# Performance work log

Hardware: AMD Instinct MI355X
Metric: run time of the kernel (lower is better)

Reference implementation:

```python
import jax, jax.numpy as jnp
import numpy as np

B, S, HID = 2, 1024, 4096
NH, NKV, D = 32, 8, 128
G = NH // NKV            # query heads per KV head (GQA group size)
WINDOW = 512             # sliding window
ROPE_BASE = 10000.0
NEG = -1e30


def setup_inputs() -> dict:
    key = jax.random.key(0)
    k0, k1, k2, k3, k4 = jax.random.split(key, 5)
    hidden_states = jax.random.normal(k0, (B, S, HID), jnp.float32)
    # rotate-half RoPE tables, width = head_dim
    inv_freq = 1.0 / (ROPE_BASE ** (jnp.arange(0, D, 2, dtype=jnp.float32) / D))
    freqs = jnp.outer(jnp.arange(S, dtype=jnp.float32), inv_freq)
    emb = jnp.concatenate([freqs, freqs], axis=-1)  # [S, D]
    cos, sin = jnp.cos(emb), jnp.sin(emb)
    qkv_out = (NH + 2 * NKV) * D  # fused QKV: 6144
    w_qkv = jax.random.normal(k1, (qkv_out, HID), jnp.float32) / np.sqrt(HID).astype(np.float32)
    b_qkv = jax.random.normal(k2, (qkv_out,), jnp.float32) * 0.01
    w_o = jax.random.normal(k3, (HID, NH * D), jnp.float32) / np.sqrt(NH * D).astype(np.float32)
    b_o = jax.random.normal(k4, (HID,), jnp.float32) * 0.01
    return dict(hidden_states=hidden_states, cos=cos, sin=sin,
                w_qkv=w_qkv, b_qkv=b_qkv, w_o=w_o, b_o=b_o)


def _rotate_half(x):
    x1, x2 = jnp.split(x, 2, axis=-1)
    return jnp.concatenate([-x2, x1], axis=-1)


def reference(hidden_states, cos, sin, w_qkv, b_qkv, w_o, b_o):
    # fused QKV projection (with bias, per attention_bias=True)
    qkv = jnp.einsum('bsh,oh->bso', hidden_states, w_qkv) + b_qkv
    q = qkv[..., : NH * D].reshape(B, S, NKV, G, D)
    k = qkv[..., NH * D : (NH + NKV) * D].reshape(B, S, NKV, D)
    v = qkv[..., (NH + NKV) * D :].reshape(B, S, NKV, D)
    # rotate-half RoPE
    c = cos[None, :, None, :]  # [1,S,1,D]
    s = sin[None, :, None, :]
    q = q * c[..., None, :] + _rotate_half(q) * s[..., None, :]
    k = k * c + _rotate_half(k) * s
    # GQA attention: scores [B, NKV, G, Sq, Sk]
    scores = jnp.einsum('bqkgd,bskd->bkgqs', q, k) / np.sqrt(D).astype(np.float32)
    i = jnp.arange(S)[:, None]
    j = jnp.arange(S)[None, :]
    mask = (j <= i) & (i - j < WINDOW)  # causal + sliding window
    scores = jnp.where(mask, scores, NEG)
    p = jax.nn.softmax(scores, axis=-1)
    attn = jnp.einsum('bkgqs,bskd->bqkgd', p, v).reshape(B, S, NH * D)
    return jnp.einsum('bsd,hd->bsh', attn, w_o) + b_o
```

## Files before the change

kernel.cpp:

```cpp
#include <hip/hip_runtime.h>
#include <hip/hip_bf16.h>

#define B_      2
#define S_      1024
#define HID     4096
#define NH      32
#define NKV     8
#define D_      128
#define G_      4
#define WINDOW  512
#define QKV_OUT 6144
#define M_TOT   2048
#define CH      32
#define VSTR    40

typedef __bf16 bf16x8 __attribute__((ext_vector_type(8)));
typedef float  f32x4  __attribute__((ext_vector_type(4)));
typedef unsigned short u16x8 __attribute__((ext_vector_type(8)));

#define AS1 __attribute__((address_space(1)))
#define AS3 __attribute__((address_space(3)))

static __device__ __forceinline__ float bf2f(unsigned short u) {
    union { unsigned int i; float f; } v; v.i = ((unsigned int)u) << 16; return v.f;
}
static __device__ __forceinline__ unsigned short f2bf(float f) {
    union { float f; unsigned int i; } v; v.f = f;
    unsigned int x = v.i;
    return (unsigned short)((x + 0x7fffu + ((x >> 16) & 1u)) >> 16);
}
static __device__ __forceinline__ void gl2lds16(const void* g, void* l) {
    __builtin_amdgcn_global_load_lds((const AS1 void*)g, (AS3 void*)l, 16, 0, 0);
}

__global__ __launch_bounds__(256)
void conv_f32_bf16(const float* __restrict__ src, unsigned short* __restrict__ dst, int n8)
{
    int i = blockIdx.x * 256 + threadIdx.x;
    if (i >= n8) return;
    const float* p = src + (size_t)i * 8;
    float4 f0 = *(const float4*)p;
    float4 f1 = *(const float4*)(p + 4);
    u16x8 h;
    h[0]=f2bf(f0.x); h[1]=f2bf(f0.y); h[2]=f2bf(f0.z); h[3]=f2bf(f0.w);
    h[4]=f2bf(f1.x); h[5]=f2bf(f1.y); h[6]=f2bf(f1.z); h[7]=f2bf(f1.w);
    *(u16x8*)&dst[(size_t)i * 8] = h;
}

template<bool C_BF16>
__global__ __launch_bounds__(256)
void gemm_bf16_bt(const unsigned short* __restrict__ A,
                  const unsigned short* __restrict__ Bw,
                  const float* __restrict__ bias,
                  void* __restrict__ Cv,
                  int M, int N, int K)
{
    __shared__ unsigned short As[128 * 32];
    __shared__ unsigned short Bs[128 * 32];

    const int tid  = threadIdx.x;
    const int m0   = blockIdx.y * 128;
    const int n0   = blockIdx.x * 128;
    const int wave = tid >> 6, lane = tid & 63;
    const int wm   = (wave >> 1) * 64;
    const int wn   = (wave & 1) * 64;
    const int lm   = lane & 15, quad = lane >> 4;

    f32x4 acc[4][4] = {};

    for (int k0 = 0; k0 < K; k0 += 32) {
        __syncthreads();
        #pragma unroll
        for (int p = 0; p < 2; ++p) {
            int chunk = tid + p * 256;
            int row   = chunk >> 2;
            int off   = (chunk & 3) * 8;
            gl2lds16(&A [(size_t)(m0 + row) * K + k0 + off], &As[chunk * 8]);
            gl2lds16(&Bw[(size_t)(n0 + row) * K + k0 + off], &Bs[chunk * 8]);
        }
        __syncthreads();

        bf16x8 afr[4], bfr[4];
        #pragma unroll
        for (int i = 0; i < 4; ++i)
            afr[i] = *(const bf16x8*)&As[(wm + i * 16 + lm) * 32 + quad * 8];
        #pragma unroll
        for (int j = 0; j < 4; ++j)
            bfr[j] = *(const bf16x8*)&Bs[(wn + j * 16 + lm) * 32 + quad * 8];

        #pragma unroll
        for (int i = 0; i < 4; ++i)
            #pragma unroll
            for (int j = 0; j < 4; ++j)
                acc[i][j] = __builtin_amdgcn_mfma_f32_16x16x32_bf16(afr[i], bfr[j], acc[i][j], 0, 0, 0);
    }

    #pragma unroll
    for (int j = 0; j < 4; ++j) {
        int col = n0 + wn + j * 16 + lm;
        float bv = bias[col];
        #pragma unroll
        for (int i = 0; i < 4; ++i) {
            int rowb = m0 + wm + i * 16 + quad * 4;
            #pragma unroll
            for (int r = 0; r < 4; ++r) {
                float val = acc[i][j][r] + bv;
                if (C_BF16)
                    ((unsigned short*)Cv)[(size_t)(rowb + r) * N + col] = f2bf(val);
                else
                    ((float*)Cv)[(size_t)(rowb + r) * N + col] = val;
            }
        }
    }
}

template<bool A_BF16, bool C_BF16>
__global__ __launch_bounds__(256)
void gemm_bt_bias(const void* __restrict__ Av,
                  const float* __restrict__ Bw,
                  const float* __restrict__ bias,
                  void* __restrict__ Cv,
                  int M, int N, int K)
{
    __shared__ unsigned short As[128 * 40];
    __shared__ unsigned short Bs[128 * 40];

    const int tid  = threadIdx.x;
    const int m0   = blockIdx.y * 128;
    const int n0   = blockIdx.x * 128;
    const int wave = tid >> 6, lane = tid & 63;
    const int wm   = (wave >> 1) * 64;
    const int wn   = (wave & 1) * 64;
    const int lm   = lane & 15, quad = lane >> 4;

    f32x4 acc[4][4] = {};

    for (int k0 = 0; k0 < K; k0 += 32) {
        __syncthreads();
        #pragma unroll
        for (int c = 0; c < 2; ++c) {
            int chunk = tid + c * 256;
            int row   = chunk >> 2;
            int off   = (chunk & 3) * 8;
            if (A_BF16) {
                *(u16x8*)&As[row * 40 + off] =
                    *(const u16x8*)&((const unsigned short*)Av)[(size_t)(m0 + row) * K + k0 + off];
            } else {
                const float* ap = &((const float*)Av)[(size_t)(m0 + row) * K + k0 + off];
                float4 f0 = *(const float4*)ap;
                float4 f1 = *(const float4*)(ap + 4);
                u16x8 h;
                h[0]=f2bf(f0.x); h[1]=f2bf(f0.y); h[2]=f2bf(f0.z); h[3]=f2bf(f0.w);
                h[4]=f2bf(f1.x); h[5]=f2bf(f1.y); h[6]=f2bf(f1.z); h[7]=f2bf(f1.w);
                *(u16x8*)&As[row * 40 + off] = h;
            }
            {
                const float* bp = &Bw[(size_t)(n0 + row) * K + k0 + off];
                float4 f0 = *(const float4*)bp;
                float4 f1 = *(const float4*)(bp + 4);
                u16x8 h;
                h[0]=f2bf(f0.x); h[1]=f2bf(f0.y); h[2]=f2bf(f0.z); h[3]=f2bf(f0.w);
                h[4]=f2bf(f1.x); h[5]=f2bf(f1.y); h[6]=f2bf(f1.z); h[7]=f2bf(f1.w);
                *(u16x8*)&Bs[row * 40 + off] = h;
            }
        }
        __syncthreads();

        bf16x8 afr[4], bfr[4];
        #pragma unroll
        for (int i = 0; i < 4; ++i)
            afr[i] = *(const bf16x8*)&As[(wm + i * 16 + lm) * 40 + quad * 8];
        #pragma unroll
        for (int j = 0; j < 4; ++j)
            bfr[j] = *(const bf16x8*)&Bs[(wn + j * 16 + lm) * 40 + quad * 8];

        #pragma unroll
        for (int i = 0; i < 4; ++i)
            #pragma unroll
            for (int j = 0; j < 4; ++j)
                acc[i][j] = __builtin_amdgcn_mfma_f32_16x16x32_bf16(afr[i], bfr[j], acc[i][j], 0, 0, 0);
    }

    #pragma unroll
    for (int j = 0; j < 4; ++j) {
        int col = n0 + wn + j * 16 + lm;
        float bv = bias[col];
        #pragma unroll
        for (int i = 0; i < 4; ++i) {
            int rowb = m0 + wm + i * 16 + quad * 4;
            #pragma unroll
            for (int r = 0; r < 4; ++r) {
                float val = acc[i][j][r] + bv;
                if (C_BF16)
                    ((unsigned short*)Cv)[(size_t)(rowb + r) * N + col] = f2bf(val);
                else
                    ((float*)Cv)[(size_t)(rowb + r) * N + col] = val;
            }
        }
    }
}

__global__ __launch_bounds__(256)
void rope_kernel(unsigned short* __restrict__ qkv,
                 const float* __restrict__ cosb,
                 const float* __restrict__ sinb)
{
    int t    = blockIdx.x * 256 + threadIdx.x;
    int d    = t & 63;
    int rest = t >> 6;
    int head = rest % 40;
    int m    = rest / 40;
    int s    = m & (S_ - 1);
    int obase = (head < NH) ? head * D_ : HID + (head - NH) * D_;
    size_t base = (size_t)m * QKV_OUT + obase;

    float x1 = bf2f(qkv[base + d]);
    float x2 = bf2f(qkv[base + d + 64]);
    float c1 = cosb[s * D_ + d];
    float s1 = sinb[s * D_ + d];
    float c2 = cosb[s * D_ + d + 64];
    float s2 = sinb[s * D_ + d + 64];
    qkv[base + d]      = f2bf(x1 * c1 - x2 * s1);
    qkv[base + d + 64] = f2bf(x2 * c2 + x1 * s2);
}

__global__ __launch_bounds__(256)
void attn_mfma(const unsigned short* __restrict__ qkv,
               unsigned short* __restrict__ attn)
{
    __shared__ unsigned short Kl[CH * 136];
    __shared__ unsigned short Vt[128 * VSTR];
    __shared__ unsigned short Pl[4][16 * 40];

    const int tid  = threadIdx.x;
    const int wave = tid >> 6, lane = tid & 63;
    const int lm   = lane & 15, quad = lane >> 4;
    const int h    = blockIdx.y;
    const int b    = blockIdx.z;
    const int kvh  = h >> 2;
    const int r0b  = blockIdx.x * 64;
    const int rw0  = r0b + wave * 16;

    const size_t qkv_b = (size_t)b * S_ * QKV_OUT;
    const float SCL = 0.12751974f;

    bf16x8 qf[4];
    {
        const unsigned short* qrow = qkv + qkv_b + (size_t)(rw0 + lm) * QKV_OUT + h * D_ + quad * 8;
        #pragma unroll
        for (int kb = 0; kb < 4; ++kb)
            qf[kb] = *(const bf16x8*)(qrow + kb * 32);
    }

    f32x4 O[8] = {};
    float mrow[4] = {-1e30f, -1e30f, -1e30f, -1e30f};
    float lrow[4] = {0.f, 0.f, 0.f, 0.f};

    const int c0   = max(0, r0b - (WINDOW - 1)) & ~(CH - 1);
    const int cend = r0b + 64 - CH;

    for (int c = c0; c <= cend; c += CH) {
        __syncthreads();
        #pragma unroll
        for (int p = 0; p < 2; ++p) {
            int idx = tid + p * 256;
            int row = idx >> 4;
            int d0  = (idx & 15) * 8;
            *(u16x8*)&Kl[row * 136 + d0] =
                *(const u16x8*)(qkv + qkv_b + (size_t)(c + row) * QKV_OUT + HID + kvh * D_ + d0);
        }
        {
            int r2 = (tid & 15) * 2;
            int d0 = (tid >> 4) * 8;
            const unsigned short* vg = qkv + qkv_b + (size_t)(c + r2) * QKV_OUT + HID + NKV * D_ + kvh * D_ + d0;
            u16x8 va = *(const u16x8*)vg;
            u16x8 vb = *(const u16x8*)(vg + QKV_OUT);
            #pragma unroll
            for (int e = 0; e < 8; ++e) {
                unsigned int pack = (unsigned int)va[e] | ((unsigned int)vb[e] << 16);
                *(unsigned int*)&Vt[(d0 + e) * VSTR + r2] = pack;
            }
        }
        __syncthreads();

        if (c + CH - 1 < rw0 - (WINDOW - 1) || c > rw0 + 15) continue;

        f32x4 s0 = {}, s1 = {};
        #pragma unroll
        for (int kb = 0; kb < 4; ++kb) {
            bf16x8 b0 = *(const bf16x8*)&Kl[lm * 136 + kb * 32 + quad * 8];
            bf16x8 b1 = *(const bf16x8*)&Kl[(16 + lm) * 136 + kb * 32 + quad * 8];
            s0 = __builtin_amdgcn_mfma_f32_16x16x32_bf16(qf[kb], b0, s0, 0, 0, 0);
            s1 = __builtin_amdgcn_mfma_f32_16x16x32_bf16(qf[kb], b1, s1, 0, 0, 0);
        }

        const int j0 = c + lm, j1 = c + 16 + lm;
        float alpha[4];
        #pragma unroll
        for (int r = 0; r < 4; ++r) {
            int row = rw0 + quad * 4 + r;
            float t0 = (j0 <= row && row - j0 < WINDOW) ? s0[r] : -3.0e38f;
            float t1 = (j1 <= row && row - j1 < WINDOW) ? s1[r] : -3.0e38f;
            float cm = fmaxf(t0, t1);
            #pragma unroll
            for (int o = 8; o >= 1; o >>= 1) cm = fmaxf(cm, __shfl_xor(cm, o, 16));
            float mnew = fmaxf(mrow[r], cm);
            float al   = exp2f((mrow[r] - mnew) * SCL);
            float p0   = exp2f((t0 - mnew) * SCL);
            float p1   = exp2f((t1 - mnew) * SCL);
            float rs   = p0 + p1;
            #pragma unroll
            for (int o = 8; o >= 1; o >>= 1) rs += __shfl_xor(rs, o, 16);
            mrow[r] = mnew;
            lrow[r] = lrow[r] * al + rs;
            alpha[r] = al;
            Pl[wave][(quad * 4 + r) * 40 + lm]      = f2bf(p0);
            Pl[wave][(quad * 4 + r) * 40 + 16 + lm] = f2bf(p1);
        }

        #pragma unroll
        for (int nt = 0; nt < 8; ++nt)
            #pragma unroll
            for (int r = 0; r < 4; ++r)
                O[nt][r] *= alpha[r];

        bf16x8 pa = *(const bf16x8*)&Pl[wave][lm * 40 + quad * 8];
        #pragma unroll
        for (int nt = 0; nt < 8; ++nt) {
            bf16x8 vbf = *(const bf16x8*)&Vt[(nt * 16 + lm) * VSTR + quad * 8];
            O[nt] = __builtin_amdgcn_mfma_f32_16x16x32_bf16(pa, vbf, O[nt], 0, 0, 0);
        }
    }

    float il[4];
    #pragma unroll
    for (int r = 0; r < 4; ++r) il[r] = 1.0f / lrow[r];
    #pragma unroll
    for (int nt = 0; nt < 8; ++nt)
        #pragma unroll
        for (int r = 0; r < 4; ++r) {
            int row = rw0 + quad * 4 + r;
            attn[(size_t)(b * S_ + row) * (NH * D_) + h * D_ + nt * 16 + lm] = f2bf(O[nt][r] * il[r]);
        }
}

extern "C" void kernel_launch(void* const* d_in, const int* in_sizes, int n_in,
                              void* d_out, int out_size, void* d_ws, size_t ws_size,
                              hipStream_t stream)
{
    const float* hidden = (const float*)d_in[0];
    const float* cosb   = (const float*)d_in[1];
    const float* sinb   = (const float*)d_in[2];
    const float* w_qkv  = (const float*)d_in[3];
    const float* b_qkv  = (const float*)d_in[4];
    const float* w_o    = (const float*)d_in[5];
    const float* b_o    = (const float*)d_in[6];
    float* out = (float*)d_out;

    unsigned char* ws = (unsigned char*)d_ws;
    const size_t QKV_B  = (size_t)M_TOT * QKV_OUT * 2;
    const size_t ATTN_B = (size_t)M_TOT * HID * 2;
    const size_t HB_B   = (size_t)M_TOT * HID * 2;
    const size_t WQ_B   = (size_t)QKV_OUT * HID * 2;
    const size_t WO_B   = (size_t)HID * HID * 2;
    const size_t NEED   = QKV_B + ATTN_B + HB_B + WQ_B;

    unsigned short* qkv_ws  = (unsigned short*)(ws);
    unsigned short* attn_ws = (unsigned short*)(ws + QKV_B);

    dim3 blk(256);

    if (ws_size >= NEED && WO_B <= HB_B + WQ_B) {
        unsigned short* hb = (unsigned short*)(ws + QKV_B + ATTN_B);
        unsigned short* wq = (unsigned short*)(ws + QKV_B + ATTN_B + HB_B);
        unsigned short* wo = (unsigned short*)(ws + QKV_B + ATTN_B);

        int n8h = M_TOT * HID / 8;
        int n8q = QKV_OUT * HID / 8;
        int n8o = HID * HID / 8;
        conv_f32_bf16<<<dim3((n8h + 255) / 256), blk, 0, stream>>>(hidden, hb, n8h);
        conv_f32_bf16<<<dim3((n8q + 255) / 256), blk, 0, stream>>>(w_qkv, wq, n8q);
        gemm_bf16_bt<true><<<dim3(QKV_OUT / 128, M_TOT / 128), blk, 0, stream>>>(
            hb, wq, b_qkv, qkv_ws, M_TOT, QKV_OUT, HID);
        rope_kernel<<<dim3((M_TOT * 40 * 64) / 256), blk, 0, stream>>>(qkv_ws, cosb, sinb);
        conv_f32_bf16<<<dim3((n8o + 255) / 256), blk, 0, stream>>>(w_o, wo, n8o);
        attn_mfma<<<dim3(S_ / 64, NH, B_), blk, 0, stream>>>(qkv_ws, attn_ws);
        gemm_bf16_bt<false><<<dim3(HID / 128, M_TOT / 128), blk, 0, stream>>>(
            attn_ws, wo, b_o, out, M_TOT, HID, NH * D_);
    } else {
        gemm_bt_bias<false, true><<<dim3(QKV_OUT / 128, M_TOT / 128), blk, 0, stream>>>(
            hidden, w_qkv, b_qkv, qkv_ws, M_TOT, QKV_OUT, HID);
        rope_kernel<<<dim3((M_TOT * 40 * 64) / 256), blk, 0, stream>>>(qkv_ws, cosb, sinb);
        attn_mfma<<<dim3(S_ / 64, NH, B_), blk, 0, stream>>>(qkv_ws, attn_ws);
        gemm_bt_bias<true, false><<<dim3(HID / 128, M_TOT / 128), blk, 0, stream>>>(
            attn_ws, w_o, b_o, out, M_TOT, HID, NH * D_);
    }
}
```

Measured before the change: 552.1 us.

## Use 256x256 eight-phase pipelined bf16 GEMM for the QKV projection

Adds a new 512-thread GEMM kernel with 256x256 output tiles, 64-wide K steps, double-buffered LDS filled by direct global-to-LDS loads, an XOR swizzle, and loads for later K tiles interleaved across four MFMA phases with explicit waitcnt and barriers. It replaces the 128x128 GEMM only for the QKV projection and is meant to raise data reuse and hide global memory latency behind MFMA work. The grid shrinks to 24x8 = 192 blocks, which may underfill the 256 CUs, and the hand-tuned waitcnt counts are fragile.

New measurement: 551.4 us. About the same (-0.1%).

```diff
diff --git a/kernel.cpp b/kernel.cpp
--- a/kernel.cpp
+++ b/kernel.cpp
@@ -45,6 +45,159 @@
     h[0]=f2bf(f0.x); h[1]=f2bf(f0.y); h[2]=f2bf(f0.z); h[3]=f2bf(f0.w);
     h[4]=f2bf(f1.x); h[5]=f2bf(f1.y); h[6]=f2bf(f1.z); h[7]=f2bf(f1.w);
     *(u16x8*)&dst[(size_t)i * 8] = h;
+}
+
+#define PHASE_TAIL(MT0, MT1)                                                           \
+    __builtin_amdgcn_sched_barrier(0);                                                 \
+    __builtin_amdgcn_s_barrier();                                                      \
+    asm volatile("s_waitcnt lgkmcnt(0)" ::: "memory");                                 \
+    __builtin_amdgcn_sched_barrier(0);                                                 \
+    __builtin_amdgcn_s_setprio(1);                                                     \
+    _Pragma("unroll")                                                                  \
+    for (int nt = 0; nt < 4; ++nt) {                                                   \
+        acc[MT0][nt] = __builtin_amdgcn_mfma_f32_16x16x32_bf16(a0[0], b[nt][0], acc[MT0][nt], 0, 0, 0); \
+        acc[MT0][nt] = __builtin_amdgcn_mfma_f32_16x16x32_bf16(a0[1], b[nt][1], acc[MT0][nt], 0, 0, 0); \
+        acc[MT1][nt] = __builtin_amdgcn_mfma_f32_16x16x32_bf16(a1[0], b[nt][0], acc[MT1][nt], 0, 0, 0); \
+        acc[MT1][nt] = __builtin_amdgcn_mfma_f32_16x16x32_bf16(a1[1], b[nt][1], acc[MT1][nt], 0, 0, 0); \
+    }                                                                                  \
+    __builtin_amdgcn_s_setprio(0);
+
+template<bool C_BF16>
+__global__ __launch_bounds__(512, 2)
+void gemm256_8ph(const unsigned short* __restrict__ A,
+                 const unsigned short* __restrict__ Bw,
+                 const float* __restrict__ bias,
+                 void* __restrict__ Cv,
+                 int M, int N, int K)
+{
+    __shared__ __attribute__((aligned(1024))) unsigned short lds[65536];
+
+    const int tid  = threadIdx.x;
+    const int lane = tid & 63;
+    const int w    = tid >> 6;
+    const int m_   = w >> 2;
+    const int n_   = w & 3;
+    const int lm   = lane & 15, quad = lane >> 4;
+    const int m0   = blockIdx.y * 256, n0 = blockIdx.x * 256;
+    const int nkt  = K >> 6;
+
+    const int lc   = lane ^ (((lane >> 5) & 1) << 1);
+    const int srow = lc >> 3;
+    const int scol = (lc & 7) * 8;
+
+    const int arow0 = m0 + m_ * 128 + n_ * 16;
+    const int arow1 = arow0 + 64;
+    const int brow  = n0 + w * 32;
+
+    const int ldsAr = m_ * 8192;
+    const int ldsA0 = ldsAr + n_ * 1024;
+    const int ldsA1 = ldsA0 + 4096;
+    const int ldsBs = 32768 + m_ * 8192 + n_ * 2048;
+    const int ldsBr = 32768 + (n_ >> 1) * 8192 + (n_ & 1) * 4096;
+
+    f32x4 acc[8][4] = {};
+
+    auto stA = [&](int T, int rp) {
+        const int k0   = T << 6;
+        const int bufo = (T & 1) << 14;
+        const int rb   = (rp ? arow1 : arow0) + srow;
+        const int lb   = (rp ? ldsA1 : ldsA0) + bufo + lane * 8;
+        gl2lds16(&A[(size_t)rb * K + k0 + scol],       &lds[lb]);
+        gl2lds16(&A[(size_t)(rb + 8) * K + k0 + scol], &lds[lb + 512]);
+    };
+    auto stB = [&](int T, int pr) {
+        const int k0   = T << 6;
+        const int bufo = (T & 1) << 14;
+        const int rb   = brow + pr * 16 + srow;
+        const int lb   = ldsBs + pr * 1024 + bufo + lane * 8;
+        gl2lds16(&Bw[(size_t)rb * K + k0 + scol],       &lds[lb]);
+        gl2lds16(&Bw[(size_t)(rb + 8) * K + k0 + scol], &lds[lb + 512]);
+    };
+    auto rdA = [&](int bufo, int mt, int ks) -> bf16x8 {
+        int e = (mt * 16 + lm) * 64 + ks * 32 + quad * 8;
+        e ^= ((e >> 8) & 1) << 4;
+        return *(const bf16x8*)&lds[bufo + ldsAr + e];
+    };
+    auto rdB = [&](int bufo, int nt, int ks) -> bf16x8 {
+        int e = (nt * 16 + lm) * 64 + ks * 32 + quad * 8;
+        e ^= ((e >> 8) & 1) << 4;
+        return *(const bf16x8*)&lds[bufo + ldsBr + e];
+    };
+
+    stB(0, 0); stB(0, 1); stA(0, 0); stA(0, 1);
+    stB(1, 0); stB(1, 1); stA(1, 0);
+    asm volatile("s_waitcnt vmcnt(6)" ::: "memory");
+    __builtin_amdgcn_sched_barrier(0);
+    __builtin_amdgcn_s_barrier();
+
+    #pragma unroll 1
+    for (int i = 0; i < nkt; ++i) {
+        const int bufo = (i & 1) << 14;
+        bf16x8 b[4][2];
+        {
+            bf16x8 a0[2], a1[2];
+            #pragma unroll
+            for (int ks = 0; ks < 2; ++ks) { a0[ks] = rdA(bufo, 0, ks); a1[ks] = rdA(bufo, 1, ks); }
+            #pragma unroll
+            for (int nt = 0; nt < 4; ++nt)
+                #pragma unroll
+                for (int ks = 0; ks < 2; ++ks) b[nt][ks] = rdB(bufo, nt, ks);
+            if (i + 1 < nkt) stA(i + 1, 1);
+            __builtin_amdgcn_sched_barrier(0);
+            asm volatile("s_waitcnt lgkmcnt(8)" ::: "memory");
+            PHASE_TAIL(0, 1)
+            __builtin_amdgcn_sched_barrier(0);
+            __builtin_amdgcn_s_barrier();
+        }
+        {
+            bf16x8 a0[2], a1[2];
+            #pragma unroll
+            for (int ks = 0; ks < 2; ++ks) { a0[ks] = rdA(bufo, 2, ks); a1[ks] = rdA(bufo, 3, ks); }
+            if (i + 2 < nkt) stB(i + 2, 0);
+            PHASE_TAIL(2, 3)
+            __builtin_amdgcn_sched_barrier(0);
+            __builtin_amdgcn_s_barrier();
+        }
+        {
+            bf16x8 a0[2], a1[2];
+            #pragma unroll
+            for (int ks = 0; ks < 2; ++ks) { a0[ks] = rdA(bufo, 4, ks); a1[ks] = rdA(bufo, 5, ks); }
+            if (i + 2 < nkt) stB(i + 2, 1);
+            PHASE_TAIL(4, 5)
+            __builtin_amdgcn_sched_barrier(0);
+            __builtin_amdgcn_s_barrier();
+        }
+        {
+            bf16x8 a0[2], a1[2];
+            #pragma unroll
+            for (int ks = 0; ks < 2; ++ks) { a0[ks] = rdA(bufo, 6, ks); a1[ks] = rdA(bufo, 7, ks); }
+            if (i + 2 < nkt) stA(i + 2, 0);
+            PHASE_TAIL(6, 7)
+            __builtin_amdgcn_sched_barrier(0);
+            if (i < nkt - 2)       { asm volatile("s_waitcnt vmcnt(6)" ::: "memory"); }
+            else if (i == nkt - 2) { asm volatile("s_waitcnt vmcnt(0)" ::: "memory"); }
+            __builtin_amdgcn_sched_barrier(0);
+            __builtin_amdgcn_s_barrier();
+        }
+    }
+
+    #pragma unroll
+    for (int nt = 0; nt < 4; ++nt) {
+        const int col = n0 + n_ * 64 + nt * 16 + lm;
+        const float bv = bias[col];
+        #pragma unroll
+        for (int mt = 0; mt < 8; ++mt) {
+            const int rowb = m0 + m_ * 128 + mt * 16 + quad * 4;
+            #pragma unroll
+            for (int r = 0; r < 4; ++r) {
+                const float val = acc[mt][nt][r] + bv;
+                if (C_BF16)
+                    ((unsigned short*)Cv)[(size_t)(rowb + r) * N + col] = f2bf(val);
+                else
+                    ((float*)Cv)[(size_t)(rowb + r) * N + col] = val;
+            }
+        }
+    }
 }
 
 template<bool C_BF16>
@@ -380,7 +533,7 @@
         int n8o = HID * HID / 8;
         conv_f32_bf16<<<dim3((n8h + 255) / 256), blk, 0, stream>>>(hidden, hb, n8h);
         conv_f32_bf16<<<dim3((n8q + 255) / 256), blk, 0, stream>>>(w_qkv, wq, n8q);
-        gemm_bf16_bt<true><<<dim3(QKV_OUT / 128, M_TOT / 128), blk, 0, stream>>>(
+        gemm256_8ph<true><<<dim3(QKV_OUT / 256, M_TOT / 256), dim3(512), 0, stream>>>(
             hb, wq, b_qkv, qkv_ws, M_TOT, QKV_OUT, HID);
         rope_kernel<<<dim3((M_TOT * 40 * 64) / 256), blk, 0, stream>>>(qkv_ws, cosb, sinb);
         conv_f32_bf16<<<dim3((n8o + 255) / 256), blk, 0, stream>>>(w_o, wo, n8o);
```
